# Kernel tuning notes

Hardware: AMD Instinct MI355X
Metric: run time of the kernel (lower is better)

Reference implementation:

```python
import jax, jax.numpy as jnp
import numpy as np

H, N, RANK = 256, 64, 1
SEQ_L = 8192


def setup_inputs() -> dict:
    key = jax.random.key(0)
    ks = jax.random.split(key, 12)
    # timescales dt in [1e-3, 1e-1] -> log_dt uniform in [log 1e-3, log 1e-1]
    log_dt = jax.random.uniform(ks[0], (H,), jnp.float32,
                                minval=np.log(1e-3), maxval=np.log(1e-1))
    def cplx(kr, ki, shape, scale=1.0):
        return (scale * jax.random.normal(kr, shape, jnp.float32),
                scale * jax.random.normal(ki, shape, jnp.float32))
    C_re, C_im = cplx(ks[1], ks[2], (1, H, N))
    B_re, B_im = cplx(ks[3], ks[4], (1, H, N))
    P_re, P_im = cplx(ks[5], ks[6], (RANK, H, N), scale=0.5)
    Q_re, Q_im = cplx(ks[7], ks[8], (RANK, H, N), scale=0.5)
    # HiPPO-NPLR-like poles: Re(w) < 0 (Hurwitz), Im(w) = pi*n ladder
    w_re = -(0.5 + 0.5 * jax.random.uniform(ks[9], (H, N), jnp.float32))
    w_im = jnp.broadcast_to(np.pi * jnp.arange(N, dtype=jnp.float32), (H, N))
    return {
        "log_dt": log_dt,
        "C_re": C_re, "C_im": C_im,
        "B_re": B_re, "B_im": B_im,
        "P_re": P_re, "P_im": P_im,
        "Q_re": Q_re, "Q_im": Q_im,
        "w_re": w_re, "w_im": w_im,
        "L": SEQ_L,
    }


def reference(log_dt, C_re, C_im, B_re, B_im, P_re, P_im, Q_re, Q_im,
              w_re, w_im, L):
    # SSKernelNPLR.forward with rate=1.0, state=None, rank=1.
    Lf = L // 2 + 1
    dt = jnp.exp(log_dt)                                   # (H,)
    w = (w_re + 1j * w_im).astype(jnp.complex64)           # (H, N)
    B = (B_re + 1j * B_im).astype(jnp.complex64)           # (1, H, N)
    C = (C_re + 1j * C_im).astype(jnp.complex64)           # (1, H, N)
    P = (P_re + 1j * P_im).astype(jnp.complex64)           # (r, H, N)
    Q = (Q_re + 1j * Q_im).astype(jnp.complex64)           # (r, H, N)

    # bilinear-transform FFT nodes
    omega = jnp.exp((-2j * jnp.pi / L) * jnp.arange(Lf)).astype(jnp.complex64)  # (Lf,)
    z = 2.0 * (1.0 - omega) / (1.0 + omega)                # (Lf,)

    wdt = w * dt[:, None]                                  # (H, N)
    Bc = jnp.concatenate([B, P], axis=0)                   # (1+r, H, N)
    Cc = jnp.concatenate([C, Q], axis=0)                   # (1+r, H, N)
    v = Bc[None, :, :, :] * Cc[:, None, :, :]              # (1+r, 1+r, H, N)

    # Cauchy kernel: r[a,b,h,l] = sum_n v[a,b,h,n] / (z[l] - wdt[h,n])
    recip = 1.0 / (z[None, None, :] - wdt[:, :, None])     # (H, N, Lf)
    r = jnp.einsum('abhn,hnl->abhl', v, recip)             # (1+r, 1+r, H, Lf)
    r = r * dt[None, None, :, None]

    # rank-1 Woodbury correction
    k_f = r[:1, :1] - r[:1, 1:] * r[1:, :1] / (1.0 + r[1:, 1:])  # (1, 1, H, Lf)
    k_f = k_f * 2.0 / (1.0 + omega)

    k = jnp.fft.irfft(k_f, n=L, axis=-1)[..., :L]          # (1, 1, H, L) real
    k_B = k[-1]                                            # (1, H, L)
    return k_B
```

## Files before the change

### kernel.cpp

```cpp
#include <hip/hip_runtime.h>
#include <hip/hip_fp16.h>
#include <math.h>

#define HDIM 256
#define NDIM 64
#define LDIM 8192
#define LF   4097
#define MDIM 4096
#define LOG2M 12
#define TW4N 3072

typedef _Float16 f16x8 __attribute__((ext_vector_type(8)));
typedef float    f32x4 __attribute__((ext_vector_type(4)));

__device__ __forceinline__ int cvt_pk_f16(float lo, float hi) {
    union { __half2 h; int i; } u;
    u.h = __floats2half2_rn(lo, hi);
    return u.i;
}

__device__ __forceinline__ int swz(int i) {
    return i ^ (((i >> 4) ^ (i >> 8)) & 15);
}

__device__ __forceinline__ int drev(unsigned x) {
    unsigned y = __brev(x) >> (32 - LOG2M);
    return (int)(((y & 0x555u) << 1) | ((y >> 1) & 0x555u));
}

__global__ __launch_bounds__(1024, 4) void fused_kernel(
    const float* __restrict__ log_dt,
    const float* __restrict__ C_re, const float* __restrict__ C_im,
    const float* __restrict__ B_re, const float* __restrict__ B_im,
    const float* __restrict__ P_re, const float* __restrict__ P_im,
    const float* __restrict__ Q_re, const float* __restrict__ Q_im,
    const float* __restrict__ w_re, const float* __restrict__ w_im,
    float2* __restrict__ out2)
{
    __shared__ float2 S[MDIM + 1];
    __shared__ float2 TW4[TW4N];

    const int h    = blockIdx.x;
    const int tid  = threadIdx.x;
    const int lane = tid & 63;
    const int wave = tid >> 6;
    const int g    = lane >> 4;
    const int m    = lane & 15;
    const float dt = expf(log_dt[h]);
    const float dtM = dt * (1.f / (float)MDIM);
    const int hb   = h * NDIM;

    for (int p = tid; p < TW4N; p += 1024) {
        float s, c;
        sincosf((6.28318530717958647692f / 4096.f) * (float)p, &s, &c);
        TW4[swz(p)] = make_float2(c, s);
    }

    if (tid < 64) {
        const float br = B_re[hb + lane], bi = B_im[hb + lane];
        const float cr = C_re[hb + lane], ci = C_im[hb + lane];
        float sr = cr * br - ci * bi;
        float si = cr * bi + ci * br;
        #pragma unroll
        for (int off = 32; off > 0; off >>= 1) {
            sr += __shfl_xor(sr, off);
            si += __shfl_xor(si, off);
        }
        if (tid == 0)
            S[swz(MDIM)] = make_float2(0.5f * dtM * sr, 0.5f * dtM * si);
    }

    float nwr_[16], nw2_[16], wi_[16];
    int   av[4][4];
    {
        const bool arow = (m < 8);
        const int  ai   = m >> 1;
        const int  c    = m & 1;
        const float* fre = (ai >= 2) ? Q_re : C_re;
        const float* fim = (ai >= 2) ? Q_im : C_im;
        const float* sre = (ai & 1) ? P_re : B_re;
        const float* sim = (ai & 1) ? P_im : B_im;
        #pragma unroll
        for (int q = 0; q < 4; ++q) {
            #pragma unroll
            for (int t = 0; t < 4; ++t) {
                const int n = hb + 16 * q + 4 * g + t;
                const float nw = -w_re[n] * dt;
                nwr_[q * 4 + t] = nw;
                nw2_[q * 4 + t] = nw * nw;
                wi_[q * 4 + t]  = w_im[n] * dt;
                float e0 = 0.f, e1 = 0.f;
                if (arow) {
                    const float fr = fre[n], fi = fim[n];
                    const float s2r = sre[n], s2i = sim[n];
                    const float vr = fr * s2r - fi * s2i;
                    const float vi = fr * s2i + fi * s2r;
                    e0 = c ? vi : vr;
                    e1 = c ? vr : -vi;
                }
                av[q][t] = cvt_pk_f16(e0, e1);
            }
        }
    }

    const int lbase = wave * 256 + m;

    float zt_[16];
    {
        float ch, sh;
        const float a0 = (3.14159265358979323846f / (float)LDIM) * (float)lbase;
        sincosf(a0, &sh, &ch);
        const float cd = 0.99998117528260114265f;
        const float sd = 0.00613588464915447536f;
        #pragma unroll
        for (int t16 = 0; t16 < 16; ++t16) {
            zt_[t16] = 2.f * sh * __builtin_amdgcn_rcpf(ch);
            const float chn = ch * cd - sh * sd;
            const float shn = sh * cd + ch * sd;
            ch = chn; sh = shn;
        }
    }

    #pragma unroll 4
    for (int t16 = 0; t16 < 16; ++t16) {
        const float zt = zt_[t16];

        f32x4 acc0 = {0.f, 0.f, 0.f, 0.f};
        f32x4 acc1 = {0.f, 0.f, 0.f, 0.f};
        #pragma unroll
        for (int q = 0; q < 4; ++q) {
            float den[4], tim[4];
            #pragma unroll
            for (int t = 0; t < 4; ++t) {
                tim[t] = zt - wi_[q * 4 + t];
                den[t] = fmaf(tim[t], tim[t], nw2_[q * 4 + t]);
            }
            const float p01 = den[0] * den[1];
            const float p23 = den[2] * den[3];
            const float rp01 = __builtin_amdgcn_rcpf(p01);
            const float rp23 = __builtin_amdgcn_rcpf(p23);
            const float rc0 = rp01 * den[1], rc1 = rp01 * den[0];
            const float rc2 = rp23 * den[3], rc3 = rp23 * den[2];

            int bv[4];
            bv[0] = cvt_pk_f16(nwr_[q * 4 + 0] * rc0, -(tim[0] * rc0));
            bv[1] = cvt_pk_f16(nwr_[q * 4 + 1] * rc1, -(tim[1] * rc1));
            bv[2] = cvt_pk_f16(nwr_[q * 4 + 2] * rc2, -(tim[2] * rc2));
            bv[3] = cvt_pk_f16(nwr_[q * 4 + 3] * rc3, -(tim[3] * rc3));

            union { int i[4]; f16x8 v; } ua, ub;
            ua.i[0] = av[q][0]; ua.i[1] = av[q][1];
            ua.i[2] = av[q][2]; ua.i[3] = av[q][3];
            ub.i[0] = bv[0]; ub.i[1] = bv[1]; ub.i[2] = bv[2]; ub.i[3] = bv[3];
            if (q < 2)
                acc0 = __builtin_amdgcn_mfma_f32_16x16x32_f16(ua.v, ub.v, acc0, 0, 0, 0);
            else
                acc1 = __builtin_amdgcn_mfma_f32_16x16x32_f16(ua.v, ub.v, acc1, 0, 0, 0);
        }
        const f32x4 acc = acc0 + acc1;

        const float o0 = __shfl_xor(acc[0], 16);
        const float o1 = __shfl_xor(acc[1], 16);
        const float o2 = __shfl_xor(acc[2], 16);
        const float o3 = __shfl_xor(acc[3], 16);
        if (lane < 16) {
            const int l = lbase + t16 * 16;
            const float numr = acc[2] * o0 - acc[3] * o1;
            const float numi = acc[2] * o1 + acc[3] * o0;
            const float d_r  = 1.f + dt * o2;
            const float d_i  = dt * o3;
            const float dd   = fmaf(d_r, d_r, d_i * d_i);
            const float rr2  = __builtin_amdgcn_rcpf(dd);
            const float cr = dt * ((numr * d_r + numi * d_i) * rr2);
            const float ci = dt * ((numi * d_r - numr * d_i) * rr2);
            const float Tr = acc[0] - cr;
            const float Ti = acc[1] - ci;
            const float Ei = 0.5f * dtM * zt;
            S[swz(l)] = make_float2(dtM * Tr - Ei * Ti, dtM * Ti + Ei * Tr);
        }
    }

    __syncthreads();

    const int l0 = tid;
    const int l1 = tid + 1024;
    const float2 Kl0 = S[swz(l0)];
    const float2 Km0 = S[swz(MDIM - l0)];
    const float2 Kl1 = S[swz(l1)];
    const float2 Km1 = S[swz(MDIM - l1)];
    float2 K2;
    if (tid == 0) K2 = S[swz(2048)];

    float w0s, w0c;
    sincosf((3.14159265358979323846f / (float)MDIM) * (float)l0, &w0s, &w0c);
    const float r2 = 0.70710678118654752440f;
    const float w1c = (w0c - w0s) * r2;
    const float w1s = (w0s + w0c) * r2;

    __syncthreads();

    {
        const float Ar = 0.5f * (Kl0.x + Km0.x);
        const float Ai = 0.5f * (Kl0.y - Km0.y);
        const float Br = 0.5f * (Kl0.x - Km0.x);
        const float Bi = 0.5f * (Kl0.y + Km0.y);
        const float Or = w0c * Br - w0s * Bi;
        const float Oi = w0c * Bi + w0s * Br;
        S[swz(drev((unsigned)l0))] = make_float2(Ar - Oi, Ai + Or);
        if (l0 > 0) {
            S[swz(drev((unsigned)(MDIM - l0)))] = make_float2(Ar + Oi, Or - Ai);
        }
    }
    {
        const float Ar = 0.5f * (Kl1.x + Km1.x);
        const float Ai = 0.5f * (Kl1.y - Km1.y);
        const float Br = 0.5f * (Kl1.x - Km1.x);
        const float Bi = 0.5f * (Kl1.y + Km1.y);
        const float Or = w1c * Br - w1s * Bi;
        const float Oi = w1c * Bi + w1s * Br;
        S[swz(drev((unsigned)l1))] = make_float2(Ar - Oi, Ai + Or);
        S[swz(drev((unsigned)(MDIM - l1)))] = make_float2(Ar + Oi, Or - Ai);
    }
    if (tid == 0) {
        S[swz(drev(2048u))] = make_float2(K2.x, -K2.y);
    }

    #pragma unroll
    for (int stage = 0; stage < 6; ++stage) {
        const int q = 1 << (2 * stage);
        __syncthreads();
        const int pos  = tid & (q - 1);
        const int base = ((tid & ~(q - 1)) << 2) | pos;
        const int f    = pos * (1024 >> (2 * stage));
        const float2 w1 = TW4[swz(f)];
        const float2 w2 = TW4[swz(2 * f)];
        const float2 w3 = TW4[swz(3 * f)];
        const float2 x0 = S[swz(base)];
        const float2 x1 = S[swz(base + q)];
        const float2 x2 = S[swz(base + 2 * q)];
        const float2 x3 = S[swz(base + 3 * q)];
        const float a1r = w1.x * x1.x - w1.y * x1.y;
        const float a1i = w1.x * x1.y + w1.y * x1.x;
        const float a2r = w2.x * x2.x - w2.y * x2.y;
        const float a2i = w2.x * x2.y + w2.y * x2.x;
        const float a3r = w3.x * x3.x - w3.y * x3.y;
        const float a3i = w3.x * x3.y + w3.y * x3.x;
        const float t0r = x0.x + a2r, t0i = x0.y + a2i;
        const float t1r = x0.x - a2r, t1i = x0.y - a2i;
        const float t2r = a1r + a3r,  t2i = a1i + a3i;
        const float t3r = a1r - a3r,  t3i = a1i - a3i;
        S[swz(base)]         = make_float2(t0r + t2r, t0i + t2i);
        S[swz(base + q)]     = make_float2(t1r - t3i, t1i + t3r);
        S[swz(base + 2 * q)] = make_float2(t0r - t2r, t0i - t2i);
        S[swz(base + 3 * q)] = make_float2(t1r + t3i, t1i - t3r);
    }
    __syncthreads();

    for (int n = tid; n < MDIM; n += 1024) {
        out2[(size_t)h * MDIM + n] = S[swz(n)];
    }
}

extern "C" void kernel_launch(void* const* d_in, const int* in_sizes, int n_in,
                              void* d_out, int out_size, void* d_ws, size_t ws_size,
                              hipStream_t stream)
{
    const float* log_dt = (const float*)d_in[0];
    const float* C_re   = (const float*)d_in[1];
    const float* C_im   = (const float*)d_in[2];
    const float* B_re   = (const float*)d_in[3];
    const float* B_im   = (const float*)d_in[4];
    const float* P_re   = (const float*)d_in[5];
    const float* P_im   = (const float*)d_in[6];
    const float* Q_re   = (const float*)d_in[7];
    const float* Q_im   = (const float*)d_in[8];
    const float* w_re   = (const float*)d_in[9];
    const float* w_im   = (const float*)d_in[10];

    float2* out2 = (float2*)d_out;

    fused_kernel<<<HDIM, 1024, 0, stream>>>(log_dt, C_re, C_im, B_re, B_im,
                                            P_re, P_im, Q_re, Q_im,
                                            w_re, w_im, out2);
}
```

Measured before the change: 36.29 us.

## Split fused kernel into parallel Cauchy kernel and separate iFFT kernel

```diff
diff --git a/kernel.cpp b/kernel.cpp
--- a/kernel.cpp
+++ b/kernel.cpp
@@ -28,19 +28,16 @@
     return (int)(((y & 0x555u) << 1) | ((y >> 1) & 0x555u));
 }
 
-__global__ __launch_bounds__(1024, 4) void fused_kernel(
+__global__ __launch_bounds__(256, 4) void cauchy_kernel(
     const float* __restrict__ log_dt,
     const float* __restrict__ C_re, const float* __restrict__ C_im,
     const float* __restrict__ B_re, const float* __restrict__ B_im,
     const float* __restrict__ P_re, const float* __restrict__ P_im,
     const float* __restrict__ Q_re, const float* __restrict__ Q_im,
     const float* __restrict__ w_re, const float* __restrict__ w_im,
-    float2* __restrict__ out2)
+    float2* __restrict__ kf)
 {
-    __shared__ float2 S[MDIM + 1];
-    __shared__ float2 TW4[TW4N];
-
-    const int h    = blockIdx.x;
+    const int h    = blockIdx.y;
     const int tid  = threadIdx.x;
     const int lane = tid & 63;
     const int wave = tid >> 6;
@@ -50,13 +47,7 @@
     const float dtM = dt * (1.f / (float)MDIM);
     const int hb   = h * NDIM;
 
-    for (int p = tid; p < TW4N; p += 1024) {
-        float s, c;
-        sincosf((6.28318530717958647692f / 4096.f) * (float)p, &s, &c);
-        TW4[swz(p)] = make_float2(c, s);
-    }
-
-    if (tid < 64) {
+    if (blockIdx.x == 0 && tid < 64) {
         const float br = B_re[hb + lane], bi = B_im[hb + lane];
         const float cr = C_re[hb + lane], ci = C_im[hb + lane];
         float sr = cr * br - ci * bi;
@@ -67,7 +58,7 @@
             si += __shfl_xor(si, off);
         }
         if (tid == 0)
-            S[swz(MDIM)] = make_float2(0.5f * dtM * sr, 0.5f * dtM * si);
+            kf[(size_t)h * LF + MDIM] = make_float2(0.5f * dtM * sr, 0.5f * dtM * si);
     }
 
     float nwr_[16], nw2_[16], wi_[16];
@@ -103,9 +94,9 @@
         }
     }
 
-    const int lbase = wave * 256 + m;
-
-    float zt_[16];
+    const int lbase = blockIdx.x * 512 + wave * 128 + m;
+
+    float zt_[8];
     {
         float ch, sh;
         const float a0 = (3.14159265358979323846f / (float)LDIM) * (float)lbase;
@@ -113,8 +104,8 @@
         const float cd = 0.99998117528260114265f;
         const float sd = 0.00613588464915447536f;
         #pragma unroll
-        for (int t16 = 0; t16 < 16; ++t16) {
-            zt_[t16] = 2.f * sh * __builtin_amdgcn_rcpf(ch);
+        for (int t8 = 0; t8 < 8; ++t8) {
+            zt_[t8] = 2.f * sh * __builtin_amdgcn_rcpf(ch);
             const float chn = ch * cd - sh * sd;
             const float shn = sh * cd + ch * sd;
             ch = chn; sh = shn;
@@ -122,8 +113,8 @@
     }
 
     #pragma unroll 4
-    for (int t16 = 0; t16 < 16; ++t16) {
-        const float zt = zt_[t16];
+    for (int t8 = 0; t8 < 8; ++t8) {
+        const float zt = zt_[t8];
 
         f32x4 acc0 = {0.f, 0.f, 0.f, 0.f};
         f32x4 acc1 = {0.f, 0.f, 0.f, 0.f};
@@ -164,7 +155,7 @@
         const float o2 = __shfl_xor(acc[2], 16);
         const float o3 = __shfl_xor(acc[3], 16);
         if (lane < 16) {
-            const int l = lbase + t16 * 16;
+            const int l = lbase + t8 * 16;
             const float numr = acc[2] * o0 - acc[3] * o1;
             const float numi = acc[2] * o1 + acc[3] * o0;
             const float d_r  = 1.f + dt * o2;
@@ -176,20 +167,33 @@
             const float Tr = acc[0] - cr;
             const float Ti = acc[1] - ci;
             const float Ei = 0.5f * dtM * zt;
-            S[swz(l)] = make_float2(dtM * Tr - Ei * Ti, dtM * Ti + Ei * Tr);
-        }
-    }
-
-    __syncthreads();
+            kf[(size_t)h * LF + l] = make_float2(dtM * Tr - Ei * Ti, dtM * Ti + Ei * Tr);
+        }
+    }
+}
+
+__global__ __launch_bounds__(1024, 4) void ifft_kernel(
+    const float2* __restrict__ kf, float2* __restrict__ out2)
+{
+    __shared__ float2 S[MDIM];
+    __shared__ float2 TW4[TW4N];
+
+    const int h   = blockIdx.x;
+    const int tid = threadIdx.x;
+    const float2* K = kf + (size_t)h * LF;
+
+    for (int p = tid; p < TW4N; p += 1024) {
+        float s, c;
+        sincosf((6.28318530717958647692f / 4096.f) * (float)p, &s, &c);
+        TW4[swz(p)] = make_float2(c, s);
+    }
 
     const int l0 = tid;
     const int l1 = tid + 1024;
-    const float2 Kl0 = S[swz(l0)];
-    const float2 Km0 = S[swz(MDIM - l0)];
-    const float2 Kl1 = S[swz(l1)];
-    const float2 Km1 = S[swz(MDIM - l1)];
-    float2 K2;
-    if (tid == 0) K2 = S[swz(2048)];
+    const float2 Kl0 = K[l0];
+    const float2 Km0 = K[MDIM - l0];
+    const float2 Kl1 = K[l1];
+    const float2 Km1 = K[MDIM - l1];
 
     float w0s, w0c;
     sincosf((3.14159265358979323846f / (float)MDIM) * (float)l0, &w0s, &w0c);
@@ -222,6 +226,7 @@
         S[swz(drev((unsigned)(MDIM - l1)))] = make_float2(Ar + Oi, Or - Ai);
     }
     if (tid == 0) {
+        const float2 K2 = K[2048];
         S[swz(drev(2048u))] = make_float2(K2.x, -K2.y);
     }
 
@@ -277,9 +282,13 @@
     const float* w_re   = (const float*)d_in[9];
     const float* w_im   = (const float*)d_in[10];
 
+    float2* kf   = (float2*)d_ws;
     float2* out2 = (float2*)d_out;
 
-    fused_kernel<<<HDIM, 1024, 0, stream>>>(log_dt, C_re, C_im, B_re, B_im,
-                                            P_re, P_im, Q_re, Q_im,
-                                            w_re, w_im, out2);
-}
+    dim3 grid1(8, HDIM);
+    cauchy_kernel<<<grid1, 256, 0, stream>>>(log_dt, C_re, C_im, B_re, B_im,
+                                             P_re, P_im, Q_re, Q_im,
+                                             w_re, w_im, kf);
+
+    ifft_kernel<<<HDIM, 1024, 0, stream>>>(kf, out2);
+}
```

New measurement: 44.93 us. +23.8%, slower.
